# Performance work log

Measured on AMD Instinct MI355X. Metric: run time of the kernel, lower is better.

Reference implementation:

```python
import jax, jax.numpy as jnp
import numpy as np

B, S, D, H = 2, 2048, 256, 8

def setup_inputs() -> dict:
    key = jax.random.key(0)
    ks = jax.random.split(key, 7)
    inputs = jax.random.normal(ks[0], (B, S, D), dtype=jnp.float32)
    timestamp = jnp.sort(jax.random.randint(ks[1], (B, S), 0, 100000, dtype=jnp.int32), axis=-1)
    wQ = jax.random.normal(ks[2], (H, D, D), dtype=jnp.float32) * 0.05
    wK = jax.random.normal(ks[3], (H, D, D), dtype=jnp.float32) * 0.05
    wV = jax.random.normal(ks[4], (H, D, D), dtype=jnp.float32) * 0.05
    wO = jax.random.normal(ks[5], (H * D, D), dtype=jnp.float32) * 0.05
    theta = jax.random.uniform(ks[6], (1, 1), dtype=jnp.float32)
    return {"inputs": inputs, "timestamp": timestamp, "wQ": wQ, "wK": wK,
            "wV": wV, "wO": wO, "theta": theta}

def reference(inputs, timestamp, wQ, wK, wV, wO, theta):
    b, s, d = inputs.shape
    # per-head projections (original loops over heads via TensorArray; vectorized here)
    Q = jnp.einsum('bsd,hde->bhse', inputs, wQ)
    K = jnp.einsum('bsd,hde->bhse', inputs, wK)
    V = jnp.einsum('bsd,hde->bhse', inputs, wV)
    exp_x = jnp.einsum('bhsd,bhtd->bhst', Q, K) / jnp.sqrt(jnp.float32(d))  # [B,H,S,S]
    x = jax.nn.softmax(exp_x, axis=-1)
    low_tri = jnp.tril(jnp.ones((s, s), dtype=jnp.float32))
    x = x * low_tri
    x = x / jnp.sum(x, axis=-1, keepdims=True)  # causal renormalized softmax

    # time-decay double-softmax branch. NOTE: the original module computes `a`
    # but returns x @ V, so `a`/`s_`/`d_` do not affect the output (dead code,
    # reproduced here for fidelity; XLA will DCE it).
    ts = timestamp.astype(jnp.float32)
    d_t = ts[:, None, :, None] - ts[:, None, None, :]  # diag(t) - t : [B,1,S,S]
    decay = (1.0 - jnp.cumsum(x, axis=-1)) * d_t * low_tri
    s_ = exp_x * jnp.exp(-(theta[0, 0] * theta[0, 0]) * decay)
    a = jax.nn.softmax(s_, axis=-1) * low_tri
    a = a / jnp.sum(a, axis=-1, keepdims=True)
    del a  # unused in original output

    ret = jnp.einsum('bhst,bhtd->bhsd', x, V)          # [B,H,S,D]
    out = ret.transpose(0, 2, 1, 3).reshape(b, s, -1)  # concat heads -> [B,S,H*D]
    return out @ wO
```

## Files before the change

### kernel.cpp

```cpp
#include <hip/hip_runtime.h>
#include <cstdint>
#include <cstddef>

#define S_LEN 2048
#define DIM   256
#define NH    8
#define NB    2
#define HDIM  (NH * DIM)

using bf16 = __bf16;
typedef __bf16 bf16x8 __attribute__((ext_vector_type(8)));
typedef __bf16 bf16x4 __attribute__((ext_vector_type(4)));
typedef float  f32x4  __attribute__((ext_vector_type(4)));

typedef const __attribute__((address_space(1))) unsigned int* as1_u32p;
typedef __attribute__((address_space(3))) unsigned int* as3_u32p;

__device__ __forceinline__ void cp16(const bf16* g, bf16* l) {
    __builtin_amdgcn_global_load_lds((as1_u32p)g, (as3_u32p)l, 16, 0, 0);
}

__global__ __launch_bounds__(256) void prep_kernel(const float* __restrict__ X,
                                                   const float* __restrict__ wQ,
                                                   const float* __restrict__ wK,
                                                   const float* __restrict__ wV,
                                                   const float* __restrict__ wO,
                                                   bf16* __restrict__ Xb,
                                                   bf16* __restrict__ WQt,
                                                   bf16* __restrict__ WKt,
                                                   bf16* __restrict__ WVt,
                                                   bf16* __restrict__ WOt)
{
    const int z = blockIdx.z;
    if (z == 4) {
        const int t = (blockIdx.y*4 + blockIdx.x)*256 + threadIdx.x;
        #pragma unroll
        for (int p = 0; p < 8; ++p) {
            const int i = (t + p*32768)*4;
            float4 v = *(const float4*)(X + i);
            bf16x4 o;
            o[0] = (bf16)v.x; o[1] = (bf16)v.y; o[2] = (bf16)v.z; o[3] = (bf16)v.w;
            *(bf16x4*)(Xb + i) = o;
        }
        return;
    }
    __shared__ float tile[64][65];
    const float* in; bf16* out; int R, C, r0, c0;
    if (z < 3) {
        const int h = blockIdx.y >> 2;
        in  = (z == 0 ? wQ : z == 1 ? wK : wV) + (size_t)h * DIM * DIM;
        out = (z == 0 ? WQt : z == 1 ? WKt : WVt) + (size_t)h * DIM * DIM;
        R = DIM; C = DIM; r0 = (blockIdx.y & 3) * 64; c0 = blockIdx.x * 64;
    } else {
        in = wO; out = WOt; R = HDIM; C = DIM;
        r0 = blockIdx.y * 64; c0 = blockIdx.x * 64;
    }
    const int tr  = threadIdx.x >> 4;
    const int tc4 = (threadIdx.x & 15) * 4;
    #pragma unroll
    for (int p = 0; p < 4; ++p) {
        int row = p * 16 + tr;
        float4 v = *(const float4*)(in + (size_t)(r0 + row) * C + c0 + tc4);
        tile[row][tc4+0] = v.x; tile[row][tc4+1] = v.y;
        tile[row][tc4+2] = v.z; tile[row][tc4+3] = v.w;
    }
    __syncthreads();
    #pragma unroll
    for (int p = 0; p < 4; ++p) {
        int orow = p * 16 + tr;
        bf16x4 o;
        #pragma unroll
        for (int j = 0; j < 4; ++j) o[j] = (bf16)tile[tc4 + j][orow];
        *(bf16x4*)(out + (size_t)(c0 + orow) * R + r0 + tc4) = o;
    }
}

template<int EPI>
__device__ __forceinline__ void gemm_tile(const bf16* __restrict__ A, const bf16* __restrict__ BT,
                                          void* __restrict__ C, bf16* As, bf16* Bs,
                                          int tm, int tn, int K, int lda, int ldb, int ldc)
{
    const int tid  = threadIdx.x;
    const int lane = tid & 63;
    const int wave = tid >> 6;
    const int wm   = (wave >> 1) << 6;
    const int wn   = (wave & 1) << 6;
    const int l16  = lane & 15;
    const int quad = lane >> 4;

    const int m0 = tm << 7, n0 = tn << 7;

    const int srow = (lane >> 2);
    const int gch  = (lane & 3) ^ (srow & 3);

    f32x4 acc[4][4] = {};

    const int ksteps = K >> 5;

    #pragma unroll
    for (int j = 0; j < 2; ++j) {
        const int g = wave*2 + j;
        cp16(A  + (size_t)(m0 + g*16 + srow)*lda + (gch << 3), As + g*512);
        cp16(BT + (size_t)(n0 + g*16 + srow)*ldb + (gch << 3), Bs + g*512);
    }

    for (int ks = 0; ks < ksteps; ++ks) {
        const int pb = ks & 1;
        asm volatile("s_waitcnt vmcnt(0)" ::: "memory");
        __syncthreads();
        if (ks + 1 < ksteps) {
            const int k1 = (ks + 1) << 5;
            #pragma unroll
            for (int j = 0; j < 2; ++j) {
                const int g = wave*2 + j;
                cp16(A  + (size_t)(m0 + g*16 + srow)*lda + k1 + (gch << 3),
                     As + (pb ^ 1)*4096 + g*512);
                cp16(BT + (size_t)(n0 + g*16 + srow)*ldb + k1 + (gch << 3),
                     Bs + (pb ^ 1)*4096 + g*512);
            }
        }
        const bf16* Ab = As + pb*4096;
        const bf16* Bb = Bs + pb*4096;
        bf16x8 af[4], bfv[4];
        #pragma unroll
        for (int i = 0; i < 4; ++i) {
            const int row = wm + i*16 + l16;
            af[i]  = *(const bf16x8*)(Ab + row*32 + ((quad ^ (l16 & 3)) << 3));
        }
        #pragma unroll
        for (int i = 0; i < 4; ++i) {
            const int row = wn + i*16 + l16;
            bfv[i] = *(const bf16x8*)(Bb + row*32 + ((quad ^ (l16 & 3)) << 3));
        }
        #pragma unroll
        for (int i = 0; i < 4; ++i)
            #pragma unroll
            for (int j = 0; j < 4; ++j)
                acc[i][j] = __builtin_amdgcn_mfma_f32_16x16x32_bf16(af[i], bfv[j], acc[i][j], 0, 0, 0);
    }

    #pragma unroll
    for (int i = 0; i < 4; ++i)
        #pragma unroll
        for (int j = 0; j < 4; ++j)
            #pragma unroll
            for (int r = 0; r < 4; ++r) {
                int mg = m0 + wm + i*16 + quad*4 + r;
                int ng = n0 + wn + j*16 + l16;
                float v = acc[i][j][r];
                if (EPI == 0)      ((bf16*)C)[(size_t)mg * ldc + ng] = (bf16)v;
                else if (EPI == 1) ((float*)C)[(size_t)mg * ldc + ng] = v;
                else               atomicAdd(&((float*)C)[(size_t)mg * ldc + ng], v);
            }
}

__global__ __launch_bounds__(256) void proj_kernel(const bf16* __restrict__ Xb,
    const bf16* __restrict__ WQt, const bf16* __restrict__ WKt, const bf16* __restrict__ WVt,
    bf16* __restrict__ Qg, bf16* __restrict__ Kg, bf16* __restrict__ VTg)
{
    __shared__ __align__(16) bf16 smem[4 * 4096];
    const int by  = blockIdx.y;
    const int mat = by >> 4;
    const int b   = (by >> 3) & 1;
    const int h   = by & 7;
    const int bx  = blockIdx.x;
    const bf16*  Xbb = Xb + (size_t)b * S_LEN * DIM;
    const size_t bh  = (size_t)(b * NH + h);
    if (mat == 0) {
        gemm_tile<0>(Xbb, WQt + (size_t)h*DIM*DIM, Qg + bh*S_LEN*DIM, smem, smem + 8192,
                     bx & 15, bx >> 4, DIM, DIM, DIM, DIM);
    } else if (mat == 1) {
        gemm_tile<0>(Xbb, WKt + (size_t)h*DIM*DIM, Kg + bh*S_LEN*DIM, smem, smem + 8192,
                     bx & 15, bx >> 4, DIM, DIM, DIM, DIM);
    } else {
        gemm_tile<0>(WVt + (size_t)h*DIM*DIM, Xbb, VTg + bh*DIM*S_LEN, smem, smem + 8192,
                     bx & 1, bx >> 1, DIM, DIM, DIM, S_LEN);
    }
}

__global__ __launch_bounds__(256) void outproj_kernel(const bf16* __restrict__ Ret,
                                                      const bf16* __restrict__ WOt,
                                                      float* __restrict__ slabs)
{
    __shared__ __align__(16) bf16 smem[4 * 4096];
    int bx = blockIdx.x;
    int t  = bx & 63;
    int kq = bx >> 6;
    gemm_tile<1>(Ret + kq*512, WOt + kq*512, slabs + (size_t)kq*4096*256,
                 smem, smem + 8192, t >> 1, t & 1, 512, HDIM, HDIM, DIM);
}

__global__ __launch_bounds__(256) void reduce_out_kernel(const float* __restrict__ slabs,
                                                         float* __restrict__ out)
{
    const size_t i = ((size_t)blockIdx.x*256 + threadIdx.x)*4;
    const size_t N = (size_t)4096*256;
    float4 a = *(const float4*)(slabs + i);
    float4 b = *(const float4*)(slabs + N + i);
    float4 c = *(const float4*)(slabs + 2*N + i);
    float4 d = *(const float4*)(slabs + 3*N + i);
    float4 w;
    w.x = a.x + b.x + c.x + d.x;
    w.y = a.y + b.y + c.y + d.y;
    w.z = a.z + b.z + c.z + d.z;
    w.w = a.w + b.w + c.w + d.w;
    *(float4*)(out + i) = w;
}

__global__ __launch_bounds__(256, 2) void attn_kernel(const bf16* __restrict__ Qg,
                                                      const bf16* __restrict__ Kg,
                                                      const bf16* __restrict__ VTg,
                                                      bf16* __restrict__ Ret,
                                                      bf16* __restrict__ Opart,
                                                      float* __restrict__ Lpart)
{
    __shared__ __align__(16) bf16 Ks [64 * 256];
    __shared__ __align__(16) bf16 VTs[256 * 64];
    __shared__ __align__(16) bf16 Ps [64 * 72];

    static const unsigned char order[63] = {
        10,29,31,32,57,60,61,
        9,25,27,28,30,48,51,52,54,55,56,58,59,62,
        8,21,23,24,26,39,42,43,45,46,47,49,50,53,
        7,17,19,20,22,33,34,36,37,38,40,41,44,
        6,13,15,16,18,35,
        5,11,12,14,
        4,3,2,1,0 };

    const int tid  = threadIdx.x;
    const int lane = tid & 63;
    const int wave = tid >> 6;
    const int l16  = lane & 15;
    const int quad = lane >> 4;
    const int cw   = wave << 6;

    const int bx  = blockIdx.x;
    const int bh  = bx & 15;
    const int bid = order[bx >> 4];
    int qt, s, nsp;
    if (bid <= 10)      { qt = bid;                    s = 0;       nsp = 1; }
    else if (bid <= 32) { int k = bid - 11; qt = 11 + (k >> 1); s = k & 1; nsp = 2; }
    else                { int k = bid - 33; int q3 = k / 3; qt = 22 + q3; s = k - 3*q3; nsp = 3; }
    const int b = bh >> 3, h = bh & 7;

    const int S2 = qt + 1;
    const int base = S2 / nsp, rem = S2 - nsp*base;
    const int kstep0 = s*base + (s < rem ? s : rem);
    const int kstep1 = kstep0 + base + (s < rem ? 1 : 0);

    const bf16* Qbh  = Qg  + (size_t)(b*NH + h) * S_LEN * DIM;
    const bf16* Kbh  = Kg  + (size_t)(b*NH + h) * S_LEN * DIM;
    const bf16* VTbh = VTg + (size_t)(b*NH + h) * DIM * S_LEN;

    const int qbase = qt*64 + wave*16;

    bf16x8 qf[8];
    #pragma unroll
    for (int kc = 0; kc < 8; ++kc)
        qf[kc] = *(const bf16x8*)(Qbh + (size_t)(qbase + l16)*DIM + kc*32 + quad*8);

    f32x4 o[16] = {};
    float l_part[4] = {0.f, 0.f, 0.f, 0.f};

    {
        const int t00 = kstep0 << 6;
        #pragma unroll
        for (int j = 0; j < 8; ++j) {
            const int sN = ((wave*8 + j) << 6) + lane;
            const int ts = sN >> 5, cs = sN & 31;
            cp16(Kbh + (size_t)(t00 + ts)*DIM + ((cs ^ (ts & 31)) << 3),
                 Ks + ((wave*8 + j) << 9));
        }
    }

    for (int step = kstep0; step < kstep1; ++step) {
        const int t0 = step << 6;
        asm volatile("s_barrier" ::: "memory");
        #pragma unroll
        for (int j = 0; j < 8; ++j) {
            const int sN = ((wave*8 + j) << 6) + lane;
            const int es = sN >> 3, cs = sN & 7;
            cp16(VTbh + (size_t)es*S_LEN + t0 + ((cs ^ (es & 7)) << 3),
                 VTs + ((wave*8 + j) << 9));
        }
        asm volatile("s_waitcnt vmcnt(8)\n\ts_barrier" ::: "memory");

        f32x4 sacc[4] = {};
        #pragma unroll
        for (int kc = 0; kc < 8; ++kc) {
            const int ch = (kc << 2) + quad;
            #pragma unroll
            for (int kt = 0; kt < 4; ++kt) {
                const int row = kt*16 + l16;
                bf16x8 kf = *(const bf16x8*)(Ks + row*256 + ((ch ^ (row & 31)) << 3));
                sacc[kt] = __builtin_amdgcn_mfma_f32_16x16x32_bf16(qf[kc], kf, sacc[kt], 0,0,0);
            }
        }

        #pragma unroll
        for (int kt = 0; kt < 4; ++kt) {
            const int tg = t0 + kt*16 + l16;
            #pragma unroll
            for (int r = 0; r < 4; ++r) {
                const int qgi = qbase + quad*4 + r;
                float p = (tg <= qgi) ? __expf(sacc[kt][r] * 0.0625f) : 0.0f;
                l_part[r] += p;
                Ps[(wave*16 + quad*4 + r)*72 + kt*16 + l16] = (bf16)p;
            }
        }
        __syncthreads();

        if (step + 1 < kstep1) {
            const int t1 = (step + 1) << 6;
            #pragma unroll
            for (int j = 0; j < 8; ++j) {
                const int sN = ((wave*8 + j) << 6) + lane;
                const int ts = sN >> 5, cs = sN & 31;
                cp16(Kbh + (size_t)(t1 + ts)*DIM + ((cs ^ (ts & 31)) << 3),
                     Ks + ((wave*8 + j) << 9));
            }
        }

        #pragma unroll
        for (int kc2 = 0; kc2 < 2; ++kc2) {
            bf16x8 pf[4];
            #pragma unroll
            for (int rt = 0; rt < 4; ++rt)
                pf[rt] = *(const bf16x8*)(Ps + (rt*16 + l16)*72 + kc2*32 + quad*8);
            #pragma unroll
            for (int ct = 0; ct < 4; ++ct) {
                const int e = cw + ct*16 + l16;
                const int g = (kc2 << 2) + quad;
                bf16x8 vf = *(const bf16x8*)(VTs + e*64 + ((g ^ (e & 7)) << 3));
                #pragma unroll
                for (int rt = 0; rt < 4; ++rt)
                    o[rt*4 + ct] = __builtin_amdgcn_mfma_f32_16x16x32_bf16(pf[rt], vf, o[rt*4 + ct], 0,0,0);
            }
        }
    }

    float lsum[4];
    #pragma unroll
    for (int r = 0; r < 4; ++r) {
        float l = l_part[r];
        l += __shfl_xor(l, 1);
        l += __shfl_xor(l, 2);
        l += __shfl_xor(l, 4);
        l += __shfl_xor(l, 8);
        lsum[r] = l;
    }

    __syncthreads();
    float* Lp = (float*)Ps;
    if (l16 == 0) {
        #pragma unroll
        for (int r = 0; r < 4; ++r) Lp[wave*16 + quad*4 + r] = lsum[r];
    }
    __syncthreads();

    if (nsp == 1) {
        #pragma unroll
        for (int rt = 0; rt < 4; ++rt)
            #pragma unroll
            for (int r = 0; r < 4; ++r) {
                const int row = rt*16 + quad*4 + r;
                const float inv = 1.0f / Lp[row];
                #pragma unroll
                for (int ct = 0; ct < 4; ++ct)
                    Ret[((size_t)b*S_LEN + qt*64 + row)*HDIM + h*DIM + cw + ct*16 + l16]
                        = (bf16)(o[rt*4 + ct][r] * inv);
            }
    } else {
        const int slotbase = (qt <= 21) ? ((qt - 11)*2 + s) : (22 + (qt - 22)*3 + s);
        const size_t slot = (size_t)bh*52 + slotbase;
        bf16*  Ob = Opart + slot * (64*256);
        float* Lb = Lpart + slot * 64;
        if (l16 == 0) {
            #pragma unroll
            for (int r = 0; r < 4; ++r) Lb[wave*16 + quad*4 + r] = lsum[r];
        }
        #pragma unroll
        for (int rt = 0; rt < 4; ++rt)
            #pragma unroll
            for (int r = 0; r < 4; ++r) {
                const int row = rt*16 + quad*4 + r;
                #pragma unroll
                for (int ct = 0; ct < 4; ++ct)
                    Ob[(size_t)row*256 + cw + ct*16 + l16] = (bf16)o[rt*4 + ct][r];
            }
    }
}

__global__ __launch_bounds__(256) void combine_kernel(const bf16* __restrict__ Opart,
                                                      const float* __restrict__ Lpart,
                                                      bf16* __restrict__ Ret)
{
    const int bx = blockIdx.x;
    const int bh = bx / 21;
    const int ti = bx - bh*21;
    const int qt = 11 + ti;
    const int n  = (qt <= 21) ? 2 : 3;
    const int slotbase = (qt <= 21) ? (qt - 11)*2 : (22 + (qt - 22)*3);
    const size_t slot0 = (size_t)bh*52 + slotbase;
    const int b = bh >> 3, h = bh & 7;
    const int row  = threadIdx.x >> 2;
    const int col0 = (threadIdx.x & 3) * 64;

    float l = 0.f;
    for (int i = 0; i < n; ++i) l += Lpart[(slot0 + i)*64 + row];
    const float inv = 1.0f / l;

    const bf16* O0 = Opart + slot0 * (64*256) + (size_t)row*256 + col0;
    const int q = qt*64 + row;
    bf16* dst = Ret + ((size_t)b*S_LEN + q)*HDIM + h*DIM + col0;
    #pragma unroll
    for (int ch = 0; ch < 8; ++ch) {
        float acc[8] = {};
        for (int i = 0; i < n; ++i) {
            bf16x8 a = *(const bf16x8*)(O0 + (size_t)i*(64*256) + ch*8);
            #pragma unroll
            for (int j = 0; j < 8; ++j) acc[j] += (float)a[j];
        }
        bf16x8 w;
        #pragma unroll
        for (int j = 0; j < 8; ++j) w[j] = (bf16)(acc[j] * inv);
        *(bf16x8*)(dst + ch*8) = w;
    }
}


extern "C" void kernel_launch(void* const* d_in, const int* in_sizes, int n_in,
                              void* d_out, int out_size, void* d_ws, size_t ws_size,
                              hipStream_t stream)
{
    (void)in_sizes; (void)n_in; (void)out_size; (void)ws_size;
    const float* X  = (const float*)d_in[0];
    const float* wQ = (const float*)d_in[2];
    const float* wK = (const float*)d_in[3];
    const float* wV = (const float*)d_in[4];
    const float* wO = (const float*)d_in[5];

    char* ws = (char*)d_ws;
    const size_t MB = 1u << 20;
    bf16*  Xb    = (bf16*)(ws + 0*MB);
    bf16*  WQt   = (bf16*)(ws + 2*MB);
    bf16*  WKt   = (bf16*)(ws + 3*MB);
    bf16*  WVt   = (bf16*)(ws + 4*MB);
    bf16*  WOt   = (bf16*)(ws + 5*MB);
    bf16*  Qg    = (bf16*)(ws + 6*MB);
    bf16*  Kg    = (bf16*)(ws + 22*MB);
    bf16*  VTg   = (bf16*)(ws + 38*MB);
    bf16*  Ret   = (bf16*)(ws + 54*MB);
    bf16*  Opart = (bf16*)(ws + 70*MB);
    float* Lpart = (float*)(ws + 98*MB);
    float* slabs = (float*)Qg;

    prep_kernel    <<<dim3(4, 32, 5), 256, 0, stream>>>(X, wQ, wK, wV, wO,
                                                        Xb, WQt, WKt, WVt, WOt);
    proj_kernel    <<<dim3(32, 48), 256, 0, stream>>>(Xb, WQt, WKt, WVt, Qg, Kg, VTg);
    attn_kernel    <<<1008,         256, 0, stream>>>(Qg, Kg, VTg, Ret, Opart, Lpart);
    combine_kernel <<<336,          256, 0, stream>>>(Opart, Lpart, Ret);
    outproj_kernel <<<256,          256, 0, stream>>>(Ret, WOt, slabs);
    reduce_out_kernel<<<1024,       256, 0, stream>>>(slabs, (float*)d_out);
}
```

Measured before the change: 184.5 us.

## Widen GEMM tiles to 128x256 with 512-thread blocks for projections

Replaces the 128x128 GEMM tile, run by 4 waves, with a 128x256 tile run by 8 waves. The A tile is now loaded once per block and shared by twice as many output columns. The QKV projection grid halves in x, and the output projection moves to an 8-way K split with 8 slabs, so the reduction kernel now sums 8 partial slabs. This cuts redundant loads of the A operand, but doubles slab write and read traffic in the output projection and changes occupancy.

```diff
diff --git a/kernel.cpp b/kernel.cpp
--- a/kernel.cpp
+++ b/kernel.cpp
@@ -76,32 +76,32 @@
 }
 
 template<int EPI>
-__device__ __forceinline__ void gemm_tile(const bf16* __restrict__ A, const bf16* __restrict__ BT,
-                                          void* __restrict__ C, bf16* As, bf16* Bs,
-                                          int tm, int tn, int K, int lda, int ldb, int ldc)
+__device__ __forceinline__ void gemm512(const bf16* __restrict__ A, const bf16* __restrict__ BT,
+                                        void* __restrict__ C, bf16* As, bf16* Bs,
+                                        int tm, int tn, int K, int lda, int ldb, int ldc)
 {
     const int tid  = threadIdx.x;
     const int lane = tid & 63;
-    const int wave = tid >> 6;
-    const int wm   = (wave >> 1) << 6;
-    const int wn   = (wave & 1) << 6;
+    const int w    = tid >> 6;
+    const int wm   = (w >> 2) << 6;
+    const int wn   = (w & 3) << 6;
     const int l16  = lane & 15;
     const int quad = lane >> 4;
 
-    const int m0 = tm << 7, n0 = tn << 7;
-
-    const int srow = (lane >> 2);
-    const int gch  = (lane & 3) ^ (srow & 3);
+    const int m0 = tm << 7, n0 = tn << 8;
+
+    const int ca = (w << 6) + lane;
+    const int ra = ca >> 2, ga = (ca & 3) ^ ((ca >> 2) & 3);
 
     f32x4 acc[4][4] = {};
-
     const int ksteps = K >> 5;
 
+    cp16(A + (size_t)(m0 + ra)*lda + (ga << 3), As + (w << 9));
     #pragma unroll
     for (int j = 0; j < 2; ++j) {
-        const int g = wave*2 + j;
-        cp16(A  + (size_t)(m0 + g*16 + srow)*lda + (gch << 3), As + g*512);
-        cp16(BT + (size_t)(n0 + g*16 + srow)*ldb + (gch << 3), Bs + g*512);
+        const int cb = ((w*2 + j) << 6) + lane;
+        const int rb = cb >> 2, gb = (cb & 3) ^ (rb & 3);
+        cp16(BT + (size_t)(n0 + rb)*ldb + (gb << 3), Bs + ((w*2 + j) << 9));
     }
 
     for (int ks = 0; ks < ksteps; ++ks) {
@@ -110,22 +110,23 @@
         __syncthreads();
         if (ks + 1 < ksteps) {
             const int k1 = (ks + 1) << 5;
+            cp16(A + (size_t)(m0 + ra)*lda + k1 + (ga << 3),
+                 As + (pb ^ 1)*4096 + (w << 9));
             #pragma unroll
             for (int j = 0; j < 2; ++j) {
-                const int g = wave*2 + j;
-                cp16(A  + (size_t)(m0 + g*16 + srow)*lda + k1 + (gch << 3),
-                     As + (pb ^ 1)*4096 + g*512);
-                cp16(BT + (size_t)(n0 + g*16 + srow)*ldb + k1 + (gch << 3),
-                     Bs + (pb ^ 1)*4096 + g*512);
+                const int cb = ((w*2 + j) << 6) + lane;
+                const int rb = cb >> 2, gb = (cb & 3) ^ (rb & 3);
+                cp16(BT + (size_t)(n0 + rb)*ldb + k1 + (gb << 3),
+                     Bs + (pb ^ 1)*8192 + ((w*2 + j) << 9));
             }
         }
         const bf16* Ab = As + pb*4096;
-        const bf16* Bb = Bs + pb*4096;
+        const bf16* Bb = Bs + pb*8192;
         bf16x8 af[4], bfv[4];
         #pragma unroll
         for (int i = 0; i < 4; ++i) {
             const int row = wm + i*16 + l16;
-            af[i]  = *(const bf16x8*)(Ab + row*32 + ((quad ^ (l16 & 3)) << 3));
+            af[i] = *(const bf16x8*)(Ab + row*32 + ((quad ^ (l16 & 3)) << 3));
         }
         #pragma unroll
         for (int i = 0; i < 4; ++i) {
@@ -148,46 +149,41 @@
                 int mg = m0 + wm + i*16 + quad*4 + r;
                 int ng = n0 + wn + j*16 + l16;
                 float v = acc[i][j][r];
-                if (EPI == 0)      ((bf16*)C)[(size_t)mg * ldc + ng] = (bf16)v;
-                else if (EPI == 1) ((float*)C)[(size_t)mg * ldc + ng] = v;
-                else               atomicAdd(&((float*)C)[(size_t)mg * ldc + ng], v);
-            }
-}
-
-__global__ __launch_bounds__(256) void proj_kernel(const bf16* __restrict__ Xb,
+                if (EPI == 0) ((bf16*)C)[(size_t)mg * ldc + ng] = (bf16)v;
+                else          ((float*)C)[(size_t)mg * ldc + ng] = v;
+            }
+}
+
+__global__ __launch_bounds__(512) void proj_kernel(const bf16* __restrict__ Xb,
     const bf16* __restrict__ WQt, const bf16* __restrict__ WKt, const bf16* __restrict__ WVt,
     bf16* __restrict__ Qg, bf16* __restrict__ Kg, bf16* __restrict__ VTg)
 {
-    __shared__ __align__(16) bf16 smem[4 * 4096];
-    const int by  = blockIdx.y;
-    const int mat = by >> 4;
-    const int b   = (by >> 3) & 1;
-    const int h   = by & 7;
-    const int bx  = blockIdx.x;
-    const bf16*  Xbb = Xb + (size_t)b * S_LEN * DIM;
-    const size_t bh  = (size_t)(b * NH + h);
-    if (mat == 0) {
-        gemm_tile<0>(Xbb, WQt + (size_t)h*DIM*DIM, Qg + bh*S_LEN*DIM, smem, smem + 8192,
-                     bx & 15, bx >> 4, DIM, DIM, DIM, DIM);
-    } else if (mat == 1) {
-        gemm_tile<0>(Xbb, WKt + (size_t)h*DIM*DIM, Kg + bh*S_LEN*DIM, smem, smem + 8192,
-                     bx & 15, bx >> 4, DIM, DIM, DIM, DIM);
+    __shared__ __align__(16) bf16 smem[3 * 8192];
+    const int y = blockIdx.y, x = blockIdx.x;
+    if (y < 32) {
+        const int mat = y >> 4, bh = y & 15;
+        const int b = bh >> 3, h = bh & 7;
+        const bf16* W = (mat ? WKt : WQt) + (size_t)h*DIM*DIM;
+        bf16*      Cg = (mat ? Kg  : Qg ) + (size_t)bh*S_LEN*DIM;
+        gemm512<0>(Xb + (size_t)b*S_LEN*DIM, W, Cg, smem, smem + 8192,
+                   x, 0, DIM, DIM, DIM, DIM);
     } else {
-        gemm_tile<0>(WVt + (size_t)h*DIM*DIM, Xbb, VTg + bh*DIM*S_LEN, smem, smem + 8192,
-                     bx & 1, bx >> 1, DIM, DIM, DIM, S_LEN);
-    }
-}
-
-__global__ __launch_bounds__(256) void outproj_kernel(const bf16* __restrict__ Ret,
+        const int bh = y - 32;
+        const int b = bh >> 3, h = bh & 7;
+        gemm512<0>(WVt + (size_t)h*DIM*DIM, Xb + (size_t)b*S_LEN*DIM,
+                   VTg + (size_t)bh*DIM*S_LEN, smem, smem + 8192,
+                   x & 1, x >> 1, DIM, DIM, DIM, S_LEN);
+    }
+}
+
+__global__ __launch_bounds__(512) void outproj_kernel(const bf16* __restrict__ Ret,
                                                       const bf16* __restrict__ WOt,
                                                       float* __restrict__ slabs)
 {
-    __shared__ __align__(16) bf16 smem[4 * 4096];
-    int bx = blockIdx.x;
-    int t  = bx & 63;
-    int kq = bx >> 6;
-    gemm_tile<1>(Ret + kq*512, WOt + kq*512, slabs + (size_t)kq*4096*256,
-                 smem, smem + 8192, t >> 1, t & 1, 512, HDIM, HDIM, DIM);
+    __shared__ __align__(16) bf16 smem[3 * 8192];
+    const int tm = blockIdx.x & 31, kq = blockIdx.x >> 5;
+    gemm512<1>(Ret + kq*256, WOt + kq*256, slabs + (size_t)kq*4096*256,
+               smem, smem + 8192, tm, 0, 256, HDIM, HDIM, DIM);
 }
 
 __global__ __launch_bounds__(256) void reduce_out_kernel(const float* __restrict__ slabs,
@@ -195,15 +191,12 @@
 {
     const size_t i = ((size_t)blockIdx.x*256 + threadIdx.x)*4;
     const size_t N = (size_t)4096*256;
-    float4 a = *(const float4*)(slabs + i);
-    float4 b = *(const float4*)(slabs + N + i);
-    float4 c = *(const float4*)(slabs + 2*N + i);
-    float4 d = *(const float4*)(slabs + 3*N + i);
-    float4 w;
-    w.x = a.x + b.x + c.x + d.x;
-    w.y = a.y + b.y + c.y + d.y;
-    w.z = a.z + b.z + c.z + d.z;
-    w.w = a.w + b.w + c.w + d.w;
+    float4 w = *(const float4*)(slabs + i);
+    #pragma unroll
+    for (int s = 1; s < 8; ++s) {
+        float4 a = *(const float4*)(slabs + (size_t)s*N + i);
+        w.x += a.x; w.y += a.y; w.z += a.z; w.w += a.w;
+    }
     *(float4*)(out + i) = w;
 }
 
@@ -457,9 +450,9 @@
 
     prep_kernel    <<<dim3(4, 32, 5), 256, 0, stream>>>(X, wQ, wK, wV, wO,
                                                         Xb, WQt, WKt, WVt, WOt);
-    proj_kernel    <<<dim3(32, 48), 256, 0, stream>>>(Xb, WQt, WKt, WVt, Qg, Kg, VTg);
+    proj_kernel    <<<dim3(16, 48), 512, 0, stream>>>(Xb, WQt, WKt, WVt, Qg, Kg, VTg);
     attn_kernel    <<<1008,         256, 0, stream>>>(Qg, Kg, VTg, Ret, Opart, Lpart);
     combine_kernel <<<336,          256, 0, stream>>>(Opart, Lpart, Ret);
-    outproj_kernel <<<256,          256, 0, stream>>>(Ret, WOt, slabs);
+    outproj_kernel <<<256,          512, 0, stream>>>(Ret, WOt, slabs);
     reduce_out_kernel<<<1024,       256, 0, stream>>>(slabs, (float*)d_out);
 }
```

Result: slower. 190.5 us (+3.2%).
